# Kernel optimization log

Measured on AMD Instinct MI355X. Metric: run time of the kernel, lower is better.

The kernel has to match this reference:

```python
import jax, jax.numpy as jnp
import numpy as np
import math

N_EMBD = 1024
N_HEAD = 16
BLOCK = 2048
SPARSITY = 0.25
B, T = 2, 2048


def _make_mask_logits(rng):
    # Replicates the patterned init in SparseMixtureAttention.__init__.
    S = BLOCK
    logits = np.empty((N_HEAD, S, S), dtype=np.float32)
    for h in range(N_HEAD):
        if h % 3 == 0:  # banded pattern (bandwidth 16)
            i = np.arange(S)
            band = (np.abs(i[:, None] - i[None, :]) <= 16)
            logits[h] = np.where(band, rng.standard_normal((S, S)) + 2.0,
                                 rng.standard_normal((S, S)) - 2.0)
        elif h % 3 == 1:  # strided pattern: every 4th column
            strided = (np.arange(S)[None, :] % 4 == 0)
            logits[h] = np.where(strided, rng.standard_normal((S, S)) + 2.0,
                                 rng.standard_normal((S, S)) - 2.0)
        else:  # random pattern with given sparsity
            rnd = rng.random((S, S)) < SPARSITY
            logits[h] = np.where(rnd, rng.standard_normal((S, S)) + 2.0,
                                 rng.standard_normal((S, S)) - 2.0)
    # keep the diagonal unmasked so no causal row is fully masked (avoids NaN rows)
    d = np.arange(S)
    logits[:, d, d] = np.abs(logits[:, d, d]) + 2.0
    return logits.astype(np.float32)


def setup_inputs() -> dict:
    key = jax.random.key(0)
    ks = jax.random.split(key, 5)
    rng = np.random.default_rng(0)
    return {
        "x": jax.random.normal(ks[0], (B, T, N_EMBD), dtype=jnp.float32),
        "mask_logits": jnp.asarray(_make_mask_logits(rng)),
        "W_attn": jax.random.normal(ks[1], (3 * N_EMBD, N_EMBD), dtype=jnp.float32) * 0.02,
        "b_attn": jnp.zeros((3 * N_EMBD,), dtype=jnp.float32),
        "W_proj": jax.random.normal(ks[2], (N_EMBD, N_EMBD), dtype=jnp.float32) * 0.02,
        "b_proj": jnp.zeros((N_EMBD,), dtype=jnp.float32),
    }


def reference(x, mask_logits, W_attn, b_attn, W_proj, b_proj):
    Bx, Tx, C = x.shape
    H = mask_logits.shape[0]
    D = C // H
    qkv = x @ W_attn.T + b_attn                       # [B,T,3C]
    q, k, v = jnp.split(qkv, 3, axis=-1)
    q = q.reshape(Bx, Tx, H, D)
    k = k.reshape(Bx, Tx, H, D)
    v = v.reshape(Bx, Tx, H, D)
    att = jnp.einsum('bthd,bshd->bhts', q, k) * (1.0 / math.sqrt(D))  # [B,H,T,T]
    # forward value of the STE mask equals the hard mask (probs - probs.detach() == 0)
    keep = jax.nn.sigmoid(mask_logits[:, :Tx, :Tx]) > 0.5             # [H,T,T]
    causal = jnp.tril(jnp.ones((Tx, Tx), dtype=bool))
    mask = causal[None, :, :] & keep                                  # [H,T,T]
    att = jnp.where(mask[None], att, -jnp.inf)
    att = jax.nn.softmax(att, axis=-1)
    y = jnp.einsum('bhts,bshd->bthd', att, v).reshape(Bx, Tx, C)
    return y @ W_proj.T + b_proj
```

## Files before the change

### kernel.cpp

```cpp
#include <hip/hip_runtime.h>
#include <hip/hip_bf16.h>
#include <stdint.h>

typedef unsigned short u16;
typedef unsigned int u32;
typedef unsigned long long u64;
typedef __attribute__((ext_vector_type(8))) short bf16x8;
typedef __attribute__((ext_vector_type(4))) float f32x4;

#define NB 2
#define NH 16
#define TT 2048
#define DD 64
#define CC 1024

__device__ __forceinline__ u16 bf16bits(float f) {
    __hip_bfloat16 h = __float2bfloat16(f);
    return __builtin_bit_cast(unsigned short, h);
}

__device__ __forceinline__ float bf2f(u16 u) {
    u32 x = (u32)u << 16;
    return __builtin_bit_cast(float, x);
}

__device__ __forceinline__ void gload_lds16(const void* g, void* l) {
    __builtin_amdgcn_global_load_lds(
        (const __attribute__((address_space(1))) void*)g,
        (__attribute__((address_space(3))) void*)l, 16, 0, 0);
}

__global__ __launch_bounds__(256) void cvt_kernel(const float* __restrict__ in,
                                                  u16* __restrict__ out, int n4) {
    int idx = blockIdx.x * blockDim.x + threadIdx.x;
    int stride = gridDim.x * blockDim.x;
    for (int i = idx; i < n4; i += stride) {
        float4 v = reinterpret_cast<const float4*>(in)[i];
        ushort4 o;
        o.x = bf16bits(v.x); o.y = bf16bits(v.y);
        o.z = bf16bits(v.z); o.w = bf16bits(v.w);
        reinterpret_cast<ushort4*>(out)[i] = o;
    }
}

__global__ __launch_bounds__(256) void mask_cvt(const float* __restrict__ ml,
                                                unsigned char* __restrict__ mb) {
    int wid = (blockIdx.x * blockDim.x + threadIdx.x) >> 6;
    int lane = threadIdx.x & 63;
    int nwaves = (gridDim.x * blockDim.x) >> 6;
    for (int row = wid; row < NH * TT; row += nwaves) {
        int i = row & (TT - 1);
        const float* src = ml + (size_t)row * TT;
        unsigned char* dst = mb + (size_t)row * (TT / 8);
        for (int c8 = lane; c8 * 8 <= i; c8 += 64) {
            const float4* p = reinterpret_cast<const float4*>(src + c8 * 8);
            float4 a = p[0];
            float4 b = p[1];
            unsigned v = 0;
            v |= (a.x > 0.f) ? 1u : 0u;
            v |= (a.y > 0.f) ? 2u : 0u;
            v |= (a.z > 0.f) ? 4u : 0u;
            v |= (a.w > 0.f) ? 8u : 0u;
            v |= (b.x > 0.f) ? 16u : 0u;
            v |= (b.y > 0.f) ? 32u : 0u;
            v |= (b.z > 0.f) ? 64u : 0u;
            v |= (b.w > 0.f) ? 128u : 0u;
            dst[c8] = (unsigned char)v;
        }
    }
}

template <int MODE>
__global__ __launch_bounds__(256) void gemm_bt(
    const u16* __restrict__ A, const u16* __restrict__ Bw,
    const float* __restrict__ bias,
    u16* __restrict__ Qb, u16* __restrict__ Kb, u16* __restrict__ Vtb,
    float* __restrict__ Cout, int Kdim) {
    const int bm = blockIdx.y * 128;
    const int bn = blockIdx.x * 128;
    const int tid = threadIdx.x;
    const int w = tid >> 6, lane = tid & 63;
    const int lrow = lane & 15, lgrp = lane >> 4;
    const int wr = (w >> 1) * 64, wc = (w & 1) * 64;

    __shared__ __align__(16) u16 ABs[2][128 * 64];
    u16* As = ABs[0];
    u16* Bs = ABs[1];

    f32x4 acc[4][4] = {};

    const int nkt = Kdim >> 6;
    for (int kt = 0; kt < nkt; ++kt) {
        const int k0 = kt << 6;
#pragma unroll
        for (int i = 0; i < 4; ++i) {
            int e = i * 2048 + tid * 8;
            int r = e >> 6, c = e & 63;
            gload_lds16(A + (size_t)(bm + r) * Kdim + k0 + c, (char*)As + i * 4096 + w * 1024);
            gload_lds16(Bw + (size_t)(bn + r) * Kdim + k0 + c, (char*)Bs + i * 4096 + w * 1024);
        }
        __syncthreads();
#pragma unroll
        for (int kk = 0; kk < 2; ++kk) {
            bf16x8 af[4], bfz[4];
#pragma unroll
            for (int i = 0; i < 4; ++i)
                af[i] = *reinterpret_cast<const bf16x8*>(&As[(wr + i * 16 + lrow) * 64 + kk * 32 + lgrp * 8]);
#pragma unroll
            for (int i = 0; i < 4; ++i)
                bfz[i] = *reinterpret_cast<const bf16x8*>(&Bs[(wc + i * 16 + lrow) * 64 + kk * 32 + lgrp * 8]);
#pragma unroll
            for (int mi = 0; mi < 4; ++mi)
#pragma unroll
                for (int ni = 0; ni < 4; ++ni)
                    acc[mi][ni] = __builtin_amdgcn_mfma_f32_16x16x32_bf16(af[mi], bfz[ni], acc[mi][ni], 0, 0, 0);
        }
        __syncthreads();
    }

    const int sec = (MODE == 0) ? (bn >> 10) : 1;

    if (MODE == 0 && sec == 2) {
        u16* Tl = &ABs[0][0];
#pragma unroll
        for (int ni = 0; ni < 4; ++ni) {
            int nl = wc + ni * 16 + lrow;
            float bv = bias[bn + nl];
#pragma unroll
            for (int mi = 0; mi < 4; ++mi) {
                int ml2 = wr + mi * 16 + lgrp * 4;
                u64 pk = 0;
#pragma unroll
                for (int j = 0; j < 4; ++j)
                    pk |= (u64)bf16bits(acc[mi][ni][j] + bv) << (16 * j);
                int byte = nl * 256 + ((ml2 * 2) ^ ((nl & 7) << 4));
                *reinterpret_cast<u64*>((char*)Tl + byte) = pk;
            }
        }
        __syncthreads();
        int r = tid >> 1, half = tid & 1;
        int h = ((bn & 1023) >> 6) + (r >> 6);
        int d = r & 63;
        int b = bm >> 11;
        u16* gdst = Vtb + (((size_t)b * NH + h) * DD + d) * TT + (bm & 2047) + half * 64;
#pragma unroll
        for (int c = 0; c < 8; ++c) {
            uint4 v = *reinterpret_cast<const uint4*>(
                (char*)Tl + r * 256 + ((half * 128 + c * 16) ^ ((r & 7) << 4)));
            *reinterpret_cast<uint4*>(gdst + c * 8) = v;
        }
        return;
    }

#pragma unroll
    for (int ni = 0; ni < 4; ++ni) {
        int n = bn + wc + ni * 16 + lrow;
        float bv = bias[n];
#pragma unroll
        for (int mi = 0; mi < 4; ++mi) {
#pragma unroll
            for (int j = 0; j < 4; ++j) {
                int m = bm + wr + mi * 16 + lgrp * 4 + j;
                float v = acc[mi][ni][j] + bv;
                if (MODE == 1) {
                    Cout[(size_t)m * 1024 + n] = v;
                } else {
                    int h = (n & 1023) >> 6;
                    int d = n & 63;
                    int b = m >> 11;
                    int t = m & 2047;
                    if (sec == 0) {
                        Qb[(((size_t)b * NH + h) * TT + t) * DD + d] =
                            bf16bits(v * (0.125f * 1.4426950408889634f));
                    } else {
                        Kb[(((size_t)b * NH + h) * TT + t) * DD + d] = bf16bits(v);
                    }
                }
            }
        }
    }
}

__global__ __launch_bounds__(256) void attn_kernel(
    const u16* __restrict__ Qb, const u16* __restrict__ Kb,
    const u16* __restrict__ Vtb, const unsigned char* __restrict__ mb,
    u16* __restrict__ att_out, u16* __restrict__ Opart,
    float* __restrict__ lpart) {
    const int bid = blockIdx.x;
    const int seg = bid >> 5;
    const int hb = bid & 31;
    const int h = hb >> 1, b = hb & 1;
    int qt, k0, k1, half = 0;
    bool split;
    if (seg < 16) {
        qt = seg; k0 = 0; k1 = qt + 1; split = false;
    } else {
        int i = seg - 16;
        qt = 16 + (i >> 1);
        half = i & 1;
        int n = qt + 1, h1 = (n + 1) >> 1;
        k0 = half ? h1 : 0;
        k1 = half ? n : h1;
        split = true;
    }

    const int tid = threadIdx.x;
    const int w = tid >> 6, lane = tid & 63;
    const int lrow = lane & 15, g = lane >> 4;

    __shared__ __align__(16) u16 Ks[2][64 * 64];
    __shared__ __align__(16) u16 Vts[2][64 * 64];
    __shared__ __align__(16) u16 Ps[4][16 * 64];

    const u16* kg_base = &Kb[((size_t)b * NH + h) * TT * DD];
    const u16* vg_base = &Vtb[((size_t)b * NH + h) * DD * TT];

    auto STAGE = [&](int bufi, int kt) {
#pragma unroll
        for (int i = 0; i < 2; ++i) {
            int e = i * 2048 + tid * 8;
            int r = e >> 6, c = e & 63;
            int cs = c ^ ((r & 7) << 3);
            gload_lds16(kg_base + (size_t)kt * 64 * DD + r * DD + cs,
                        (char*)Ks[bufi] + i * 4096 + w * 1024);
            gload_lds16(vg_base + kt * 64 + (size_t)r * TT + cs,
                        (char*)Vts[bufi] + i * 4096 + w * 1024);
        }
    };

    const int qrow_g = qt * 64 + w * 16 + lrow;
    const int rswz = (lrow & 7) << 4;

    bf16x8 qf[2];
#pragma unroll
    for (int kk = 0; kk < 2; ++kk)
        qf[kk] = *reinterpret_cast<const bf16x8*>(
            &Qb[(((size_t)b * NH + h) * TT + qrow_g) * DD + kk * 32 + g * 8]);

    f32x4 oacc[4] = {};
    float l_run = 0.f;

    const unsigned char* mrow_base = mb + ((size_t)h * TT + qrow_g) * (TT / 8);
    char* PsW = (char*)&Ps[w][0];

    STAGE(0, k0);
    __syncthreads();
    int buf = 0;

#pragma unroll 1
    for (int kt = k0; kt < k1; ++kt) {
        u64 mw = *reinterpret_cast<const u64*>(mrow_base + kt * 8);
        if (kt + 1 < k1) STAGE(buf ^ 1, kt + 1);

        f32x4 s[4] = {};
        __builtin_amdgcn_s_setprio(1);
#pragma unroll
        for (int kk = 0; kk < 2; ++kk)
#pragma unroll
            for (int nt = 0; nt < 4; ++nt) {
                bf16x8 kf = *reinterpret_cast<const bf16x8*>(
                    (char*)Ks[buf] + (((nt * 16 + lrow) * 128 + (kk * 32 + g * 8) * 2) ^ rswz));
                s[nt] = __builtin_amdgcn_mfma_f32_16x16x32_bf16(kf, qf[kk], s[nt], 0, 0, 0);
            }
        __builtin_amdgcn_s_setprio(0);

        u64 mws = mw >> (g * 4);
        u32 mlo = (u32)mws, mhi = (u32)(mws >> 32);
        float rs = 0.f;
        if (kt == qt) {
#pragma unroll
            for (int nt = 0; nt < 4; ++nt)
#pragma unroll
                for (int j = 0; j < 4; ++j) {
                    int bi = nt * 16 + j;
                    bool keep = (((bi < 32 ? mlo : mhi) >> (bi & 31)) & 1) &&
                                (kt * 64 + nt * 16 + g * 4 + j <= qrow_g);
                    float p = keep ? exp2f(s[nt][j]) : 0.f;
                    rs += p;
                    s[nt][j] = p;
                }
        } else {
#pragma unroll
            for (int nt = 0; nt < 4; ++nt)
#pragma unroll
                for (int j = 0; j < 4; ++j) {
                    int bi = nt * 16 + j;
                    bool keep = ((bi < 32 ? mlo : mhi) >> (bi & 31)) & 1;
                    float p = keep ? exp2f(s[nt][j]) : 0.f;
                    rs += p;
                    s[nt][j] = p;
                }
        }
        rs += __shfl_xor(rs, 16);
        rs += __shfl_xor(rs, 32);
        l_run += rs;

#pragma unroll
        for (int nt = 0; nt < 4; ++nt)
#pragma unroll
            for (int t = 0; t < 2; ++t) {
                u32 pk = (u32)bf16bits(s[nt][2 * t]) |
                         ((u32)bf16bits(s[nt][2 * t + 1]) << 16);
                int byte = (lrow * 128 + (nt * 16 + g * 4 + 2 * t) * 2) ^ rswz;
                *reinterpret_cast<u32*>(PsW + byte) = pk;
            }

        __builtin_amdgcn_s_setprio(1);
#pragma unroll
        for (int kk = 0; kk < 2; ++kk) {
            bf16x8 pf = *reinterpret_cast<const bf16x8*>(
                PsW + ((lrow * 128 + (kk * 32 + g * 8) * 2) ^ rswz));
#pragma unroll
            for (int dt = 0; dt < 4; ++dt) {
                bf16x8 vf = *reinterpret_cast<const bf16x8*>(
                    (char*)Vts[buf] + (((dt * 16 + lrow) * 128 + (kk * 32 + g * 8) * 2) ^ rswz));
                oacc[dt] = __builtin_amdgcn_mfma_f32_16x16x32_bf16(pf, vf, oacc[dt], 0, 0, 0);
            }
        }
        __builtin_amdgcn_s_setprio(0);

        __syncthreads();
        buf ^= 1;
    }

    if (!split) {
        float lb[4];
#pragma unroll
        for (int j = 0; j < 4; ++j)
            lb[j] = __shfl(l_run, (lane & 48) + g * 4 + j);
#pragma unroll
        for (int dt = 0; dt < 4; ++dt)
#pragma unroll
            for (int j = 0; j < 4; ++j) {
                int t = qt * 64 + w * 16 + g * 4 + j;
                float o = oacc[dt][j] / lb[j];
                att_out[((size_t)b * TT + t) * CC + h * DD + dt * 16 + lrow] = bf16bits(o);
            }
    } else {
        const int slot = (hb * 16 + (qt - 16)) * 2 + half;
        u16* Op = Opart + (size_t)slot * 4096;
#pragma unroll
        for (int dt = 0; dt < 4; ++dt)
#pragma unroll
            for (int j = 0; j < 4; ++j) {
                int row = w * 16 + g * 4 + j;
                Op[row * 64 + dt * 16 + lrow] = bf16bits(oacc[dt][j]);
            }
        if (g == 0) lpart[(size_t)slot * 64 + w * 16 + lrow] = l_run;
    }
}

__global__ __launch_bounds__(256) void combine_kernel(
    const u16* __restrict__ Opart, const float* __restrict__ lpart,
    u16* __restrict__ att_out) {
    const int cid = blockIdx.x;
    const int hb = cid >> 4;
    const int h = hb >> 1, b = hb & 1;
    const int qt = 16 + (cid & 15);
    const int t = threadIdx.x;
    const int row = t >> 2, c0 = (t & 3) << 4;

    const u16* p0 = Opart + ((size_t)cid * 2) * 4096 + row * 64 + c0;
    const u16* p1 = p0 + 4096;
    float l = lpart[(size_t)cid * 128 + row] + lpart[(size_t)cid * 128 + 64 + row];
    float inv = 1.0f / l;

    u16 ov[16];
#pragma unroll
    for (int i = 0; i < 16; ++i)
        ov[i] = bf16bits((bf2f(p0[i]) + bf2f(p1[i])) * inv);

    u16* dst = att_out + ((size_t)b * TT + qt * 64 + row) * CC + h * DD + c0;
#pragma unroll
    for (int i = 0; i < 2; ++i)
        reinterpret_cast<uint4*>(dst)[i] = reinterpret_cast<const uint4*>(ov)[i];
}

extern "C" void kernel_launch(void* const* d_in, const int* in_sizes, int n_in,
                              void* d_out, int out_size, void* d_ws, size_t ws_size,
                              hipStream_t stream) {
    const float* x = (const float*)d_in[0];
    const float* mask_logits = (const float*)d_in[1];
    const float* W_attn = (const float*)d_in[2];
    const float* b_attn = (const float*)d_in[3];
    const float* W_proj = (const float*)d_in[4];
    const float* b_proj = (const float*)d_in[5];
    float* out = (float*)d_out;

    char* ws = (char*)d_ws;
    u16* xb    = (u16*)(ws + 0);
    u16* Wa    = (u16*)(ws + (8u << 20));
    u16* Qb    = (u16*)(ws + (16u << 20));
    u16* Kb    = (u16*)(ws + (24u << 20));
    u16* Vtb   = (u16*)(ws + (32u << 20));
    u16* att   = (u16*)(ws + (40u << 20));
    u16* Wp    = (u16*)(ws + (48u << 20));
    float* lpart = (float*)(ws + (50u << 20));
    u16* Opart = (u16*)(ws + (8u << 20));
    unsigned char* mbits = (unsigned char*)(ws + 0);

    cvt_kernel<<<2048, 256, 0, stream>>>(x, xb, NB * TT * CC / 4);
    cvt_kernel<<<2048, 256, 0, stream>>>(W_attn, Wa, 3 * CC * CC / 4);
    cvt_kernel<<<1024, 256, 0, stream>>>(W_proj, Wp, CC * CC / 4);

    gemm_bt<0><<<dim3(24, 32), 256, 0, stream>>>(xb, Wa, b_attn, Qb, Kb, Vtb, nullptr, CC);
    mask_cvt<<<1024, 256, 0, stream>>>(mask_logits, mbits);
    attn_kernel<<<1536, 256, 0, stream>>>(Qb, Kb, Vtb, mbits, att, Opart, lpart);
    combine_kernel<<<512, 256, 0, stream>>>(Opart, lpart, att);
    gemm_bt<1><<<dim3(8, 32), 256, 0, stream>>>(att, Wp, b_proj, nullptr, nullptr, nullptr, out, CC);
}
```

Baseline: 175.3 us.

## Fold mask bit-packing into QKV GEMM launch as extra blocks

The separate mask_cvt launch is removed. Its work runs in 12 extra grid rows of the QKV GEMM (24x12 blocks, 1056 waves), so the bandwidth-bound mask packing overlaps the compute-bound GEMM and one launch disappears. Workspace offsets are rearranged so the mask bits no longer alias buffers the GEMM reads. The extra blocks compete with GEMM blocks for CUs and bandwidth, and fewer waves handle the mask rows.

```diff
diff --git a/kernel.cpp b/kernel.cpp
--- a/kernel.cpp
+++ b/kernel.cpp
@@ -43,42 +43,44 @@
     }
 }
 
-__global__ __launch_bounds__(256) void mask_cvt(const float* __restrict__ ml,
-                                                unsigned char* __restrict__ mb) {
-    int wid = (blockIdx.x * blockDim.x + threadIdx.x) >> 6;
-    int lane = threadIdx.x & 63;
-    int nwaves = (gridDim.x * blockDim.x) >> 6;
-    for (int row = wid; row < NH * TT; row += nwaves) {
-        int i = row & (TT - 1);
-        const float* src = ml + (size_t)row * TT;
-        unsigned char* dst = mb + (size_t)row * (TT / 8);
-        for (int c8 = lane; c8 * 8 <= i; c8 += 64) {
-            const float4* p = reinterpret_cast<const float4*>(src + c8 * 8);
-            float4 a = p[0];
-            float4 b = p[1];
-            unsigned v = 0;
-            v |= (a.x > 0.f) ? 1u : 0u;
-            v |= (a.y > 0.f) ? 2u : 0u;
-            v |= (a.z > 0.f) ? 4u : 0u;
-            v |= (a.w > 0.f) ? 8u : 0u;
-            v |= (b.x > 0.f) ? 16u : 0u;
-            v |= (b.y > 0.f) ? 32u : 0u;
-            v |= (b.z > 0.f) ? 64u : 0u;
-            v |= (b.w > 0.f) ? 128u : 0u;
-            dst[c8] = (unsigned char)v;
-        }
-    }
-}
-
 template <int MODE>
 __global__ __launch_bounds__(256) void gemm_bt(
     const u16* __restrict__ A, const u16* __restrict__ Bw,
     const float* __restrict__ bias,
     u16* __restrict__ Qb, u16* __restrict__ Kb, u16* __restrict__ Vtb,
-    float* __restrict__ Cout, int Kdim) {
+    float* __restrict__ Cout, const float* __restrict__ ml,
+    unsigned char* __restrict__ mbout, int Kdim) {
+    const int tid = threadIdx.x;
+
+    if (MODE == 0 && blockIdx.y >= 32) {
+        int wid = ((blockIdx.y - 32) * 24 + blockIdx.x) * 4 + (tid >> 6);
+        int lane = tid & 63;
+#pragma unroll 1
+        for (int row = wid; row < NH * TT; row += 1056) {
+            int i = row & (TT - 1);
+            const float* src = ml + (size_t)row * TT;
+            unsigned char* dst = mbout + (size_t)row * (TT / 8);
+            for (int c8 = lane; c8 * 8 <= i; c8 += 64) {
+                const float4* p = reinterpret_cast<const float4*>(src + c8 * 8);
+                float4 a = p[0];
+                float4 bb = p[1];
+                unsigned v = 0;
+                v |= (a.x > 0.f) ? 1u : 0u;
+                v |= (a.y > 0.f) ? 2u : 0u;
+                v |= (a.z > 0.f) ? 4u : 0u;
+                v |= (a.w > 0.f) ? 8u : 0u;
+                v |= (bb.x > 0.f) ? 16u : 0u;
+                v |= (bb.y > 0.f) ? 32u : 0u;
+                v |= (bb.z > 0.f) ? 64u : 0u;
+                v |= (bb.w > 0.f) ? 128u : 0u;
+                dst[c8] = (unsigned char)v;
+            }
+        }
+        return;
+    }
+
     const int bm = blockIdx.y * 128;
     const int bn = blockIdx.x * 128;
-    const int tid = threadIdx.x;
     const int w = tid >> 6, lane = tid & 63;
     const int lrow = lane & 15, lgrp = lane >> 4;
     const int wr = (w >> 1) * 64, wc = (w & 1) * 64;
@@ -390,22 +392,23 @@
     char* ws = (char*)d_ws;
     u16* xb    = (u16*)(ws + 0);
     u16* Wa    = (u16*)(ws + (8u << 20));
+    u16* Wp    = (u16*)(ws + (14u << 20));
     u16* Qb    = (u16*)(ws + (16u << 20));
     u16* Kb    = (u16*)(ws + (24u << 20));
     u16* Vtb   = (u16*)(ws + (32u << 20));
     u16* att   = (u16*)(ws + (40u << 20));
-    u16* Wp    = (u16*)(ws + (48u << 20));
-    float* lpart = (float*)(ws + (50u << 20));
-    u16* Opart = (u16*)(ws + (8u << 20));
-    unsigned char* mbits = (unsigned char*)(ws + 0);
+    unsigned char* mbits = (unsigned char*)(ws + (48u << 20));
+    u16* Opart = (u16*)(ws + 0);
+    float* lpart = (float*)(ws + (8u << 20));
 
     cvt_kernel<<<2048, 256, 0, stream>>>(x, xb, NB * TT * CC / 4);
     cvt_kernel<<<2048, 256, 0, stream>>>(W_attn, Wa, 3 * CC * CC / 4);
     cvt_kernel<<<1024, 256, 0, stream>>>(W_proj, Wp, CC * CC / 4);
 
-    gemm_bt<0><<<dim3(24, 32), 256, 0, stream>>>(xb, Wa, b_attn, Qb, Kb, Vtb, nullptr, CC);
-    mask_cvt<<<1024, 256, 0, stream>>>(mask_logits, mbits);
+    gemm_bt<0><<<dim3(24, 44), 256, 0, stream>>>(xb, Wa, b_attn, Qb, Kb, Vtb,
+                                                 nullptr, mask_logits, mbits, CC);
     attn_kernel<<<1536, 256, 0, stream>>>(Qb, Kb, Vtb, mbits, att, Opart, lpart);
     combine_kernel<<<512, 256, 0, stream>>>(Opart, lpart, att);
-    gemm_bt<1><<<dim3(8, 32), 256, 0, stream>>>(att, Wp, b_proj, nullptr, nullptr, nullptr, out, CC);
-}
+    gemm_bt<1><<<dim3(8, 32), 256, 0, stream>>>(att, Wp, b_proj, nullptr, nullptr, nullptr,
+                                                out, nullptr, nullptr, CC);
+}
```

Measured after the change: 185.6 us. 1.06x slower.
